# Performance work log

Hardware: AMD Instinct MI355X
Metric: run time of the kernel (lower is better)

Reference implementation:

```python
import jax, jax.numpy as jnp
import numpy as np

B, C, H, W = 2, 512, 32, 32
HEADS = 8      # attention heads
GROUPS = 8     # offset groups (defaults to heads)
DH = 64        # dim_head
DF = 4         # downsample_factor
OFF_SCALE = 4.0
EPS = 1e-5


def _bn(t, gamma, beta):
    # eval-mode BatchNorm2d with running_mean=0, running_var=1
    s = gamma / jnp.sqrt(1.0 + EPS)
    return t * s[None, :, None, None] + beta[None, :, None, None]


def _gconv1x1(t, w):
    # grouped 1x1 conv (bias-free); w: (GROUPS, out_per_group, in_per_group)
    b, c, h, ww = t.shape
    o = jnp.einsum('bgci,goc->bgoi', t.reshape(b, GROUPS, c // GROUPS, h * ww), w)
    return o.reshape(b, GROUPS * w.shape[1], h, ww)


def _grid_sample(img, grid):
    # F.grid_sample: bilinear, padding_mode='zeros', align_corners=False
    # img: (N,Ci,Hi,Wi); grid: (N,Hg,Wg,2), grid[...,0]=x, grid[...,1]=y in [-1,1]
    N, Ci, Hi, Wi = img.shape
    gx = (grid[..., 0] + 1.0) * (Wi / 2.0) - 0.5
    gy = (grid[..., 1] + 1.0) * (Hi / 2.0) - 0.5
    x0 = jnp.floor(gx)
    y0 = jnp.floor(gy)
    wx = gx - x0
    wy = gy - y0

    def gather(im, ix, iy):
        valid = (ix >= 0) & (ix < Wi) & (iy >= 0) & (iy < Hi)
        ixc = jnp.clip(ix, 0, Wi - 1).astype(jnp.int32)
        iyc = jnp.clip(iy, 0, Hi - 1).astype(jnp.int32)
        return im[:, iyc, ixc] * valid[None].astype(im.dtype)

    def sample_one(im, x0, y0, wx, wy):
        v00 = gather(im, x0, y0)
        v01 = gather(im, x0 + 1, y0)
        v10 = gather(im, x0, y0 + 1)
        v11 = gather(im, x0 + 1, y0 + 1)
        wx = wx[None]
        wy = wy[None]
        return (v00 * (1 - wx) * (1 - wy) + v01 * wx * (1 - wy)
                + v10 * (1 - wx) * wy + v11 * wx * wy)

    return jax.vmap(sample_one)(img, x0, y0, wx, wy)


def _forward(x, bn1_g, bn1_b, bn2_g, bn2_b, qw, kw, vw, out_w, out_b,
             off_dw_w, off_dw_b, off_pw_w,
             cpb_w1, cpb_b1, cpb_w2, cpb_b2, cpb_w3, cpb_b3,
             mlp_w1, mlp_b1, mlp_w2, mlp_b2):
    b = x.shape[0]
    xn = _bn(x, bn1_g, bn1_b)
    # ---- deformable attention ----
    q = _gconv1x1(xn, qw)                                   # (b, 512, H, W)
    qg = q.reshape(b * GROUPS, DH, H, W)
    # to_offsets: depthwise conv k=6, s=4, p=1 -> GELU -> 1x1(64->2) -> tanh * offset_scale
    off = jax.lax.conv_general_dilated(
        qg, off_dw_w, (DF, DF), ((1, 1), (1, 1)),
        dimension_numbers=('NCHW', 'OIHW', 'NCHW'), feature_group_count=DH)
    off = jax.nn.gelu(off + off_dw_b[None, :, None, None], approximate=False)
    off = jnp.tanh(jnp.einsum('bchw,oc->bohw', off, off_pw_w)) * OFF_SCALE   # (b*G, 2, Hd, Wd)
    Hd, Wd = off.shape[-2], off.shape[-1]
    gy, gx = jnp.meshgrid(jnp.arange(Hd, dtype=x.dtype), jnp.arange(Wd, dtype=x.dtype), indexing='ij')
    vx = gx[None] + off[:, 0]
    vy = gy[None] + off[:, 1]
    # normalize_grid (lucidrains): first comp by (Hd-1), second by (Wd-1)
    nx = 2.0 * vx / max(Hd - 1, 1) - 1.0
    ny = 2.0 * vy / max(Wd - 1, 1) - 1.0
    vgrid_scaled = jnp.stack((nx, ny), axis=-1)             # (b*G, Hd, Wd, 2)
    kv = _grid_sample(xn.reshape(b * GROUPS, DH, H, W), vgrid_scaled)
    kv = kv.reshape(b, GROUPS * DH, Hd, Wd)
    k = _gconv1x1(kv, kw)
    v = _gconv1x1(kv, vw)
    scale = DH ** -0.5
    qh = q.reshape(b, HEADS, DH, H * W).transpose(0, 1, 3, 2) * scale    # (b,h,i,d)
    kh = k.reshape(b, HEADS, DH, Hd * Wd).transpose(0, 1, 3, 2)          # (b,h,j,d)
    vh = v.reshape(b, HEADS, DH, Hd * Wd).transpose(0, 1, 3, 2)
    # continuous relative position bias (CPB)
    qgy, qgx = jnp.meshgrid(jnp.arange(H, dtype=x.dtype), jnp.arange(W, dtype=x.dtype), indexing='ij')
    grid_q = jnp.stack((2.0 * qgx / max(H - 1, 1) - 1.0,
                        2.0 * qgy / max(W - 1, 1) - 1.0), axis=-1).reshape(1, H * W, 2)
    grid_kv = vgrid_scaled.reshape(b * GROUPS, Hd * Wd, 2)
    pos = grid_q[:, :, None, :] - grid_kv[:, None, :, :]    # (b*G, i, j, 2)
    bias = jnp.sign(pos) * jnp.log1p(jnp.abs(pos))
    bias = jax.nn.relu(bias @ cpb_w1 + cpb_b1)
    bias = jax.nn.relu(bias @ cpb_w2 + cpb_b2)
    bias = (bias @ cpb_w3 + cpb_b3).reshape(b, GROUPS, H * W, Hd * Wd)   # heads//groups == 1
    sim = jnp.einsum('bhid,bhjd->bhij', qh, kh) + bias
    attn = jax.nn.softmax(sim, axis=-1)
    out = jnp.einsum('bhij,bhjd->bhid', attn, vh)
    out = out.transpose(0, 1, 3, 2).reshape(b, HEADS * DH, H, W)
    out = jnp.einsum('bchw,oc->bohw', out, out_w) + out_b[None, :, None, None]
    x = x + out
    # ---- conv1x1 MLP ----
    xn2 = _bn(x, bn2_g, bn2_b)
    h1 = jax.nn.gelu(jnp.einsum('bchw,oc->bohw', xn2, mlp_w1) + mlp_b1[None, :, None, None],
                     approximate=False)
    return x + jnp.einsum('bchw,oc->bohw', h1, mlp_w2) + mlp_b2[None, :, None, None]


def setup_inputs():
    ks = jax.random.split(jax.random.key(0), 16)
    w = lambda k, shape: jax.random.normal(k, shape, dtype=jnp.float32) * 0.02
    return {
        'x': jax.random.normal(ks[0], (B, C, H, W), dtype=jnp.float32),
        'bn1_g': jnp.ones((C,), jnp.float32),
        'bn1_b': jnp.zeros((C,), jnp.float32),
        'bn2_g': jnp.ones((C,), jnp.float32),
        'bn2_b': jnp.zeros((C,), jnp.float32),
        'qw': w(ks[1], (GROUPS, DH, C // GROUPS)),
        'kw': w(ks[2], (GROUPS, DH, C // GROUPS)),
        'vw': w(ks[3], (GROUPS, DH, C // GROUPS)),
        'out_w': w(ks[4], (C, HEADS * DH)),
        'out_b': jnp.zeros((C,), jnp.float32),
        'off_dw_w': w(ks[5], (DH, 1, 6, 6)),
        'off_dw_b': jnp.zeros((DH,), jnp.float32),
        'off_pw_w': w(ks[6], (2, DH)),
        'cpb_w1': w(ks[7], (2, 128)),
        'cpb_b1': jnp.zeros((128,), jnp.float32),
        'cpb_w2': w(ks[8], (128, 128)),
        'cpb_b2': jnp.zeros((128,), jnp.float32),
        'cpb_w3': w(ks[9], (128, 1)),
        'cpb_b3': jnp.zeros((1,), jnp.float32),
        'mlp_w1': w(ks[10], (4 * C, C)),
        'mlp_b1': jnp.zeros((4 * C,), jnp.float32),
        'mlp_w2': w(ks[11], (C, 4 * C)),
        'mlp_b2': jnp.zeros((C,), jnp.float32),
    }


def reference(x, bn1_g, bn1_b, bn2_g, bn2_b, qw, kw, vw, out_w, out_b,
              off_dw_w, off_dw_b, off_pw_w,
              cpb_w1, cpb_b1, cpb_w2, cpb_b2, cpb_w3, cpb_b3,
              mlp_w1, mlp_b1, mlp_w2, mlp_b2):
    return _forward(x, bn1_g, bn1_b, bn2_g, bn2_b, qw, kw, vw, out_w, out_b,
                    off_dw_w, off_dw_b, off_pw_w,
                    cpb_w1, cpb_b1, cpb_w2, cpb_b2, cpb_w3, cpb_b3,
                    mlp_w1, mlp_b1, mlp_w2, mlp_b2)
```

## Files before the change

kernel.cpp:

```cpp
#include <hip/hip_runtime.h>
#include <hip/hip_bf16.h>
#include <math.h>

#define BB 2
#define CC 512
#define HH 32
#define WW 32
#define HWP 1024
#define GG 8
#define DH 64
#define HD 8
#define WD 8
#define JJ 64
#define BG 16
#define EPS 1e-5f

typedef __attribute__((ext_vector_type(8))) short short8;
typedef __attribute__((ext_vector_type(4))) short s16x4;
typedef __attribute__((ext_vector_type(4))) float f32x4;
typedef __attribute__((ext_vector_type(4))) unsigned short u16x4;
typedef __attribute__((ext_vector_type(4))) unsigned int u32x4;

static __device__ __forceinline__ short f2bf(float x) {
    unsigned u = __builtin_bit_cast(unsigned, x);
    u += 0x7FFFu + ((u >> 16) & 1u);
    return (short)(u >> 16);
}
static __device__ __forceinline__ float bf2f(unsigned short h) {
    return __builtin_bit_cast(float, (unsigned)h << 16);
}

__global__ void k_wpack(const float* __restrict__ qw, const float* __restrict__ ow,
                        const float* __restrict__ w1, const float* __restrict__ w2,
                        const float* __restrict__ cw2, unsigned short* __restrict__ wp,
                        unsigned short* __restrict__ w2p) {
    int idx = blockIdx.x * 256 + threadIdx.x;
    if (idx < 2392064) {
        float v;
        if (idx < 32768) v = qw[idx];
        else if (idx < 294912) v = ow[idx - 32768];
        else if (idx < 1343488) v = w1[idx - 294912];
        else v = w2[idx - 1343488];
        wp[idx] = (unsigned short)f2bf(v);
    } else if (idx < 2408448) {
        int i2 = idx - 2392064;
        int k = i2 >> 7, n = i2 & 127;
        int dest = ((((n >> 4) * 4 + (k >> 5)) * 64) + (((k >> 3) & 3) * 16) + (n & 15)) * 8 + (k & 7);
        w2p[dest] = (unsigned short)f2bf(cw2[i2]);
    }
}

__global__ __launch_bounds__(256) void k_qgemm(
    const float* __restrict__ x, const float* __restrict__ g1,
    const float* __restrict__ b1, const unsigned short* __restrict__ qwp,
    unsigned short* __restrict__ qt) {
    __shared__ __align__(16) short As[64][72];
    __shared__ __align__(16) short Bs[64][72];
    int blk = blockIdx.x;
    int bg = blk >> 4, nt = blk & 15;
    int b = bg >> 3, g = bg & 7;
    int i0 = nt * 64;
    int tid = threadIdx.x, lane = tid & 63, wv = tid >> 6;
    int wm = (wv >> 1) * 32, wn = (wv & 1) * 32;
    int l15 = lane & 15, quad = lane >> 4;
    const float invs = 1.0f / sqrtf(1.0f + EPS);
    {
        int c4 = (tid & 15) * 4;
        int ob = tid >> 4;
#pragma unroll
        for (int p = 0; p < 4; p++) {
            int o = ob + p * 16;
            u16x4 v = *(const u16x4*)(qwp + (size_t)(g * 64 + o) * 64 + c4);
            *(u16x4*)&As[o][c4] = v;
        }
    }
    {
        int i4 = (tid & 15) * 4;
        int cb = tid >> 4;
#pragma unroll
        for (int p = 0; p < 4; p++) {
            int c = cb + p * 16;
            f32x4 v = *(const f32x4*)(x + (size_t)(b * CC + g * 64 + c) * HWP + i0 + i4);
            float sc = g1[g * 64 + c] * invs;
            float sh = b1[g * 64 + c];
            Bs[i4 + 0][c] = f2bf(fmaf(v.x, sc, sh));
            Bs[i4 + 1][c] = f2bf(fmaf(v.y, sc, sh));
            Bs[i4 + 2][c] = f2bf(fmaf(v.z, sc, sh));
            Bs[i4 + 3][c] = f2bf(fmaf(v.w, sc, sh));
        }
    }
    __syncthreads();
    f32x4 acc[2][2];
#pragma unroll
    for (int a = 0; a < 2; a++)
#pragma unroll
        for (int c = 0; c < 2; c++) acc[a][c] = (f32x4){0.f, 0.f, 0.f, 0.f};
#pragma unroll
    for (int ks = 0; ks < 2; ks++) {
        short8 af0 = *(const short8*)&As[wm + l15][ks * 32 + quad * 8];
        short8 af1 = *(const short8*)&As[wm + 16 + l15][ks * 32 + quad * 8];
        short8 bf0 = *(const short8*)&Bs[wn + l15][ks * 32 + quad * 8];
        short8 bf1 = *(const short8*)&Bs[wn + 16 + l15][ks * 32 + quad * 8];
        acc[0][0] = __builtin_amdgcn_mfma_f32_16x16x32_bf16(af0, bf0, acc[0][0], 0, 0, 0);
        acc[0][1] = __builtin_amdgcn_mfma_f32_16x16x32_bf16(af0, bf1, acc[0][1], 0, 0, 0);
        acc[1][0] = __builtin_amdgcn_mfma_f32_16x16x32_bf16(af1, bf0, acc[1][0], 0, 0, 0);
        acc[1][1] = __builtin_amdgcn_mfma_f32_16x16x32_bf16(af1, bf1, acc[1][1], 0, 0, 0);
    }
    __syncthreads();
#pragma unroll
    for (int im = 0; im < 2; im++)
#pragma unroll
        for (int r = 0; r < 4; r++) {
            int m = wm + im * 16 + quad * 4 + r;
#pragma unroll
            for (int in_ = 0; in_ < 2; in_++) {
                int n = wn + in_ * 16 + l15;
                As[n][m] = f2bf(acc[im][in_][r]);
            }
        }
    __syncthreads();
    {
        int n = tid >> 2;
        int c0 = (tid & 3) * 16;
        short8 a = *(const short8*)&As[n][c0];
        short8 c = *(const short8*)&As[n][c0 + 8];
        unsigned short* dst = qt + ((size_t)bg * 1024 + i0 + n) * 64 + c0;
        *(short8*)dst = a;
        *(short8*)(dst + 8) = c;
    }
}

__global__ __launch_bounds__(64) void k_offskv(
    const unsigned short* __restrict__ qt, const float* __restrict__ dww,
    const float* __restrict__ dwb, const float* __restrict__ pw,
    const float* __restrict__ x, const float* __restrict__ g1,
    const float* __restrict__ b1, const float* __restrict__ kw,
    const float* __restrict__ vw, float* __restrict__ vgrid,
    float* __restrict__ kk, float* __restrict__ vv) {
    __shared__ float sm[64];
    int blk = blockIdx.x;
    int bg = blk >> 6;
    int hd = (blk >> 3) & 7;
    int wd = blk & 7;
    int g = bg & 7, b = bg >> 3;
    int ch = threadIdx.x;
    const unsigned short* qb = qt + (size_t)bg * 65536;
    float acc = 0.f;
#pragma unroll
    for (int kh = 0; kh < 6; kh++) {
        int hin = hd * 4 - 1 + kh;
        if (hin < 0 || hin >= HH) continue;
#pragma unroll
        for (int kw_ = 0; kw_ < 6; kw_++) {
            int win = wd * 4 - 1 + kw_;
            if (win < 0 || win >= WW) continue;
            acc = fmaf(bf2f(qb[(hin * WW + win) * 64 + ch]), dww[ch * 36 + kh * 6 + kw_], acc);
        }
    }
    acc += dwb[ch];
    float ge = 0.5f * acc * (1.0f + erff(acc * 0.7071067811865475f));
    float p0 = ge * pw[ch];
    float p1 = ge * pw[64 + ch];
#pragma unroll
    for (int off = 32; off; off >>= 1) {
        p0 += __shfl_xor(p0, off);
        p1 += __shfl_xor(p1, off);
    }
    float nx = 2.0f * ((float)wd + tanhf(p0) * 4.0f) / 7.0f - 1.0f;
    float ny = 2.0f * ((float)hd + tanhf(p1) * 4.0f) / 7.0f - 1.0f;
    if (ch == 0) {
        vgrid[blk * 2] = nx;
        vgrid[blk * 2 + 1] = ny;
    }
    {
        int cg = g * 64 + ch;
        const float invs = 1.0f / sqrtf(1.0f + EPS);
        float s = g1[cg] * invs;
        float bv = b1[cg];
        float gx = (nx + 1.0f) * 16.0f - 0.5f;
        float gy = (ny + 1.0f) * 16.0f - 0.5f;
        float x0f = floorf(gx), y0f = floorf(gy);
        float wx = gx - x0f, wy = gy - y0f;
        int x0 = (int)x0f, y0 = (int)y0f;
        const float* im = x + (size_t)(b * CC + cg) * HWP;
        float sx = 0.f, sw = 0.f;
        float w00 = (1 - wx) * (1 - wy), w01 = wx * (1 - wy);
        float w10 = (1 - wx) * wy, w11 = wx * wy;
        if (x0 >= 0 && x0 < WW && y0 >= 0 && y0 < HH)                 { sx += w00 * im[y0 * WW + x0];           sw += w00; }
        if (x0 + 1 >= 0 && x0 + 1 < WW && y0 >= 0 && y0 < HH)         { sx += w01 * im[y0 * WW + x0 + 1];       sw += w01; }
        if (x0 >= 0 && x0 < WW && y0 + 1 >= 0 && y0 + 1 < HH)         { sx += w10 * im[(y0 + 1) * WW + x0];     sw += w10; }
        if (x0 + 1 >= 0 && x0 + 1 < WW && y0 + 1 >= 0 && y0 + 1 < HH) { sx += w11 * im[(y0 + 1) * WW + x0 + 1]; sw += w11; }
        sm[ch] = s * sx + bv * sw;
    }
    __syncthreads();
    int j = blk & 63;
    const float* kwr = kw + (size_t)(g * 64 + ch) * 64;
    const float* vwr = vw + (size_t)(g * 64 + ch) * 64;
    float ak = 0.f, av = 0.f;
#pragma unroll
    for (int c = 0; c < 64; c++) {
        float tv = sm[c];
        ak = fmaf(tv, kwr[c], ak);
        av = fmaf(tv, vwr[c], av);
    }
    kk[(size_t)bg * 4096 + j * 64 + ch] = ak;
    vv[(size_t)bg * 4096 + j * 64 + ch] = av;
}

__global__ __launch_bounds__(256) void k_cpb(
    const float* __restrict__ vgrid, const unsigned short* __restrict__ w2p,
    const float* __restrict__ w1, const float* __restrict__ b1,
    const float* __restrict__ b2, const float* __restrict__ w3,
    const float* __restrict__ b3, float* __restrict__ bias) {
    __shared__ __align__(16) short w2fs[16384];
    int tid = threadIdx.x;
    {
        const u32x4* src = (const u32x4*)w2p;
        u32x4* dst = (u32x4*)w2fs;
        for (int c = tid; c < 2048; c += 256) dst[c] = src[c];
    }
    float bias3 = b3[0];
    __syncthreads();

    int lane = tid & 63;
    int wv = tid >> 6;
    int l15 = lane & 15;
    int quad = lane >> 4;

#pragma unroll 1
    for (int it = 0; it < 4; it++) {
        int p = (blockIdx.x * 4 + it) * 4 + wv;
        int cofs = (int)((unsigned)p >> 20);
        int bg = p >> 11;
        int i = (p >> 1) & 1023;
        int jbase = (p & 1) * 32;
        int hi = i >> 5, wi = i & 31;
        float qx = 2.0f * (float)wi / 31.0f - 1.0f;
        float qy = 2.0f * (float)hi / 31.0f - 1.0f;

        int jA = jbase + l15;
        float gkxA = vgrid[(bg * 64 + jA) * 2];
        float gkyA = vgrid[(bg * 64 + jA) * 2 + 1];
        float gkxB = vgrid[(bg * 64 + jA + 16) * 2];
        float gkyB = vgrid[(bg * 64 + jA + 16) * 2 + 1];
        float p0 = qx - gkxA, p1 = qy - gkyA;
        float s0a = copysignf(log1pf(fabsf(p0)), p0);
        float s1a = copysignf(log1pf(fabsf(p1)), p1);
        p0 = qx - gkxB; p1 = qy - gkyB;
        float s0b = copysignf(log1pf(fabsf(p0)), p0);
        float s1b = copysignf(log1pf(fabsf(p1)), p1);

        short8 hA[4], hB[4];
#pragma unroll
        for (int kc = 0; kc < 4; kc++) {
            f32x4 cu0 = *(const f32x4*)(w1 + cofs + kc * 32 + quad * 8);
            f32x4 cu1 = *(const f32x4*)(w1 + cofs + kc * 32 + quad * 8 + 4);
            f32x4 cv0 = *(const f32x4*)(w1 + cofs + 128 + kc * 32 + quad * 8);
            f32x4 cv1 = *(const f32x4*)(w1 + cofs + 128 + kc * 32 + quad * 8 + 4);
            f32x4 cb0 = *(const f32x4*)(b1 + cofs + kc * 32 + quad * 8);
            f32x4 cb1 = *(const f32x4*)(b1 + cofs + kc * 32 + quad * 8 + 4);
            u32x4 pa, pb;
#pragma unroll
            for (int j2 = 0; j2 < 4; j2++) {
                int e0 = 2 * j2, e1 = 2 * j2 + 1;
                float u0 = (e0 < 4) ? cu0[e0] : cu1[e0 - 4];
                float u1 = (e1 < 4) ? cu0[e1] : cu1[e1 - 4];
                float v0 = (e0 < 4) ? cv0[e0] : cv1[e0 - 4];
                float v1 = (e1 < 4) ? cv0[e1] : cv1[e1 - 4];
                float c0 = (e0 < 4) ? cb0[e0] : cb1[e0 - 4];
                float c1 = (e1 < 4) ? cb0[e1] : cb1[e1 - 4];
                unsigned a0 = __builtin_bit_cast(unsigned,
                    fmaxf(fmaf(s0a, u0, fmaf(s1a, v0, c0)), 0.f)) + 0x8000u;
                unsigned a1 = __builtin_bit_cast(unsigned,
                    fmaxf(fmaf(s0a, u1, fmaf(s1a, v1, c1)), 0.f)) + 0x8000u;
                pa[j2] = __builtin_amdgcn_perm(a1, a0, 0x07060302);
                unsigned b0 = __builtin_bit_cast(unsigned,
                    fmaxf(fmaf(s0b, u0, fmaf(s1b, v0, c0)), 0.f)) + 0x8000u;
                unsigned b1_ = __builtin_bit_cast(unsigned,
                    fmaxf(fmaf(s0b, u1, fmaf(s1b, v1, c1)), 0.f)) + 0x8000u;
                pb[j2] = __builtin_amdgcn_perm(b1_, b0, 0x07060302);
            }
            hA[kc] = __builtin_bit_cast(short8, pa);
            hB[kc] = __builtin_bit_cast(short8, pb);
        }

        float psumA = 0.f, psumB = 0.f;
#pragma unroll 2
        for (int nt = 0; nt < 8; nt++) {
            f32x4 accA = (f32x4){0.f, 0.f, 0.f, 0.f};
            f32x4 accB = (f32x4){0.f, 0.f, 0.f, 0.f};
#pragma unroll
            for (int kc = 0; kc < 4; kc++) {
                short8 af = *(const short8*)(w2fs + (((nt * 4 + kc) * 64) + lane) * 8);
                accA = __builtin_amdgcn_mfma_f32_16x16x32_bf16(af, hA[kc], accA, 0, 0, 0);
                accB = __builtin_amdgcn_mfma_f32_16x16x32_bf16(af, hB[kc], accB, 0, 0, 0);
            }
            f32x4 b2q = *(const f32x4*)(b2 + cofs + nt * 16 + quad * 4);
            f32x4 w3q = *(const f32x4*)(w3 + cofs + nt * 16 + quad * 4);
#pragma unroll
            for (int r = 0; r < 4; r++) {
                psumA = fmaf(fmaxf(accA[r] + b2q[r], 0.f), w3q[r], psumA);
                psumB = fmaf(fmaxf(accB[r] + b2q[r], 0.f), w3q[r], psumB);
            }
        }
        psumA += __shfl_xor(psumA, 16);
        psumA += __shfl_xor(psumA, 32);
        psumB += __shfl_xor(psumB, 16);
        psumB += __shfl_xor(psumB, 32);
        if (quad == 0) {
            bias[(size_t)(p * 2 + 0) * 16 + l15] = psumA + bias3;
            bias[(size_t)(p * 2 + 1) * 16 + l15] = psumB + bias3;
        }
    }
}

__global__ __launch_bounds__(256) void k_attn(
    const unsigned short* __restrict__ qt, const float* __restrict__ kk,
    const float* __restrict__ vv, const float* __restrict__ bias,
    unsigned short* __restrict__ ao) {
    __shared__ __align__(16) short Ks[64][72];
    __shared__ __align__(16) short Vt[64][72];
    __shared__ __align__(16) short Qs[64][72];
    __shared__ __align__(16) short Ps[4][16][72];
    int blk = blockIdx.x;
    int bg = blk >> 4;
    int chunk = blk & 15;
    int i0 = chunk * 64;
    int b = bg >> 3, g = bg & 7;
    int tid = threadIdx.x, lane = tid & 63, wv = tid >> 6;
    int l15 = lane & 15, quad = lane >> 4;

    const float* kbase = kk + (size_t)bg * 4096;
    const float* vbase = vv + (size_t)bg * 4096;
#pragma unroll
    for (int it = 0; it < 4; it++) {
        int e4 = it * 1024 + tid * 4;
        int j = e4 >> 6, d = e4 & 63;
        f32x4 k4 = *(const f32x4*)(kbase + e4);
        s16x4 s = {f2bf(k4.x), f2bf(k4.y), f2bf(k4.z), f2bf(k4.w)};
        *(s16x4*)&Ks[j][d] = s;
        f32x4 v4 = *(const f32x4*)(vbase + e4);
        Vt[d + 0][j] = f2bf(v4.x);
        Vt[d + 1][j] = f2bf(v4.y);
        Vt[d + 2][j] = f2bf(v4.z);
        Vt[d + 3][j] = f2bf(v4.w);
    }
    {
        const unsigned short* qtb = qt + ((size_t)bg * 1024 + i0) * 64;
#pragma unroll
        for (int it = 0; it < 4; it++) {
            int e4 = it * 1024 + tid * 4;
            int i = e4 >> 6, d = e4 & 63;
            u16x4 v = *(const u16x4*)(qtb + e4);
            *(u16x4*)&Qs[i][d] = v;
        }
    }
    __syncthreads();

    int iw = wv * 16;
    f32x4 Sacc[4];
#pragma unroll
    for (int nt = 0; nt < 4; nt++) Sacc[nt] = (f32x4){0.f, 0.f, 0.f, 0.f};
#pragma unroll
    for (int ks = 0; ks < 2; ks++) {
        short8 aq = *(const short8*)&Qs[iw + l15][quad * 8 + ks * 32];
#pragma unroll
        for (int nt = 0; nt < 4; nt++) {
            short8 bk = *(const short8*)&Ks[nt * 16 + l15][quad * 8 + ks * 32];
            Sacc[nt] = __builtin_amdgcn_mfma_f32_16x16x32_bf16(aq, bk, Sacc[nt], 0, 0, 0);
        }
    }
    const float* bp = bias + ((size_t)bg * 1024 + i0 + iw + quad * 4) * 64 + l15;
    float Sv[4][4];
#pragma unroll
    for (int nt = 0; nt < 4; nt++)
#pragma unroll
        for (int r = 0; r < 4; r++)
            Sv[nt][r] = fmaf(Sacc[nt][r], 0.125f, bp[r * 64 + nt * 16]);
#pragma unroll
    for (int r = 0; r < 4; r++) {
        float m = fmaxf(fmaxf(Sv[0][r], Sv[1][r]), fmaxf(Sv[2][r], Sv[3][r]));
        m = fmaxf(m, __shfl_xor(m, 1));
        m = fmaxf(m, __shfl_xor(m, 2));
        m = fmaxf(m, __shfl_xor(m, 4));
        m = fmaxf(m, __shfl_xor(m, 8));
        float l = 0.f;
#pragma unroll
        for (int nt = 0; nt < 4; nt++) { Sv[nt][r] = expf(Sv[nt][r] - m); l += Sv[nt][r]; }
        l += __shfl_xor(l, 1);
        l += __shfl_xor(l, 2);
        l += __shfl_xor(l, 4);
        l += __shfl_xor(l, 8);
        float inv = 1.0f / l;
#pragma unroll
        for (int nt = 0; nt < 4; nt++)
            Ps[wv][quad * 4 + r][nt * 16 + l15] = f2bf(Sv[nt][r] * inv);
    }
    f32x4 Oacc[4];
#pragma unroll
    for (int nt = 0; nt < 4; nt++) Oacc[nt] = (f32x4){0.f, 0.f, 0.f, 0.f};
#pragma unroll
    for (int ks = 0; ks < 2; ks++) {
        short8 ap = *(const short8*)&Ps[wv][l15][quad * 8 + ks * 32];
#pragma unroll
        for (int nt = 0; nt < 4; nt++) {
            short8 bv = *(const short8*)&Vt[nt * 16 + l15][quad * 8 + ks * 32];
            Oacc[nt] = __builtin_amdgcn_mfma_f32_16x16x32_bf16(ap, bv, Oacc[nt], 0, 0, 0);
        }
    }
    __syncthreads();
#pragma unroll
    for (int nt = 0; nt < 4; nt++) {
        s16x4 o4 = {f2bf(Oacc[nt][0]), f2bf(Oacc[nt][1]), f2bf(Oacc[nt][2]), f2bf(Oacc[nt][3])};
        *(s16x4*)&Qs[nt * 16 + l15][iw + quad * 4] = o4;
    }
    __syncthreads();
    {
        int d = tid >> 2;
        int ic = (tid & 3) * 16;
        short8 a = *(const short8*)&Qs[d][ic];
        short8 c = *(const short8*)&Qs[d][ic + 8];
        unsigned short* dst = ao + (size_t)(b * CC + g * 64 + d) * HWP + i0 + ic;
        *(short8*)dst = a;
        *(short8*)(dst + 8) = c;
    }
}

template<int EPI, int KD, int BK, int MT>
__global__ __launch_bounds__(256) void k_gemm(
    const unsigned short* __restrict__ A, const unsigned short* __restrict__ Bh,
    const float* __restrict__ resid, const float* __restrict__ bias,
    void* __restrict__ outp, unsigned short* __restrict__ out2,
    const float* __restrict__ bns, const float* __restrict__ bnb) {
    constexpr int MM = MT * 64;
    __shared__ __align__(16) short As[64][BK + 8];
    __shared__ __align__(16) short Bs[64][BK + 8];
    int tid = threadIdx.x;
    int blk = blockIdx.x;
    int mt = blk & (MT - 1);
    int nb = blk / MT;
    int bb = nb >> 4, nt = nb & 15;
    int m0 = mt * 64, i0 = nt * 64;
    int lane = tid & 63, wv = tid >> 6;
    int wm = (wv >> 1) * 32, wn = (wv & 1) * 32;
    int l15 = lane & 15, quad = lane >> 4;
    const unsigned short* Af = A + (size_t)m0 * KD;
    const float invs = 1.0f / sqrtf(1.0f + EPS);

    f32x4 acc[2][2];
#pragma unroll
    for (int a = 0; a < 2; a++)
#pragma unroll
        for (int c = 0; c < 2; c++) acc[a][c] = (f32x4){0.f, 0.f, 0.f, 0.f};

    for (int k0 = 0; k0 < KD; k0 += BK) {
        __syncthreads();
        {
            int kk4 = (tid & (BK / 4 - 1)) * 4;
            int myb = tid / (BK / 4);
            constexpr int RP = 256 / (BK / 4);
#pragma unroll
            for (int p = 0; p < 64 / RP; p++) {
                int my = myb + p * RP;
                u16x4 v = *(const u16x4*)(Af + (size_t)my * KD + k0 + kk4);
                *(u16x4*)&As[my][kk4] = v;
            }
        }
        {
            int i4 = (tid & 15) * 4;
            int kyb = tid >> 4;
#pragma unroll
            for (int p = 0; p < BK / 16; p++) {
                int ky = kyb + p * 16;
                size_t goff = (size_t)bb * KD * HWP + (size_t)(k0 + ky) * HWP + i0 + i4;
                u16x4 v = *(const u16x4*)(Bh + goff);
                Bs[i4 + 0][ky] = (short)v.x;
                Bs[i4 + 1][ky] = (short)v.y;
                Bs[i4 + 2][ky] = (short)v.z;
                Bs[i4 + 3][ky] = (short)v.w;
            }
        }
        __syncthreads();
#pragma unroll
        for (int ks = 0; ks < BK / 32; ks++) {
            short8 af0 = *(const short8*)&As[wm + l15][ks * 32 + quad * 8];
            short8 af1 = *(const short8*)&As[wm + 16 + l15][ks * 32 + quad * 8];
            short8 bf0 = *(const short8*)&Bs[wn + l15][ks * 32 + quad * 8];
            short8 bf1 = *(const short8*)&Bs[wn + 16 + l15][ks * 32 + quad * 8];
            acc[0][0] = __builtin_amdgcn_mfma_f32_16x16x32_bf16(af0, bf0, acc[0][0], 0, 0, 0);
            acc[0][1] = __builtin_amdgcn_mfma_f32_16x16x32_bf16(af0, bf1, acc[0][1], 0, 0, 0);
            acc[1][0] = __builtin_amdgcn_mfma_f32_16x16x32_bf16(af1, bf0, acc[1][0], 0, 0, 0);
            acc[1][1] = __builtin_amdgcn_mfma_f32_16x16x32_bf16(af1, bf1, acc[1][1], 0, 0, 0);
        }
    }

    float* outF = (float*)outp;
    unsigned short* outH = (unsigned short*)outp;
#pragma unroll
    for (int im = 0; im < 2; im++) {
#pragma unroll
        for (int r = 0; r < 4; r++) {
            int m = m0 + wm + im * 16 + quad * 4 + r;
            float bv = bias[m];
#pragma unroll
            for (int in_ = 0; in_ < 2; in_++) {
                int n = i0 + wn + in_ * 16 + l15;
                size_t idx = ((size_t)bb * MM + m) * HWP + n;
                float v = acc[im][in_][r] + bv;
                if constexpr (EPI == 1) {
                    float ge = 0.5f * v * (1.0f + erff(v * 0.7071067811865475f));
                    outH[idx] = (unsigned short)f2bf(ge);
                } else if constexpr (EPI == 3) {
                    float vr = v + resid[idx];
                    outF[idx] = vr;
                    out2[idx] = (unsigned short)f2bf(fmaf(vr, bns[m] * invs, bnb[m]));
                } else {
                    outF[idx] = v + resid[idx];
                }
            }
        }
    }
}

extern "C" void kernel_launch(void* const* d_in, const int* in_sizes, int n_in,
                              void* d_out, int out_size, void* d_ws, size_t ws_size,
                              hipStream_t stream) {
    const float* x      = (const float*)d_in[0];
    const float* bn1_g  = (const float*)d_in[1];
    const float* bn1_b  = (const float*)d_in[2];
    const float* bn2_g  = (const float*)d_in[3];
    const float* bn2_b  = (const float*)d_in[4];
    const float* qw     = (const float*)d_in[5];
    const float* kw     = (const float*)d_in[6];
    const float* vw     = (const float*)d_in[7];
    const float* out_w  = (const float*)d_in[8];
    const float* out_b  = (const float*)d_in[9];
    const float* off_dw_w = (const float*)d_in[10];
    const float* off_dw_b = (const float*)d_in[11];
    const float* off_pw_w = (const float*)d_in[12];
    const float* cpb_w1 = (const float*)d_in[13];
    const float* cpb_b1 = (const float*)d_in[14];
    const float* cpb_w2 = (const float*)d_in[15];
    const float* cpb_b2 = (const float*)d_in[16];
    const float* cpb_w3 = (const float*)d_in[17];
    const float* cpb_b3 = (const float*)d_in[18];
    const float* mlp_w1 = (const float*)d_in[19];
    const float* mlp_b1 = (const float*)d_in[20];
    const float* mlp_w2 = (const float*)d_in[21];
    const float* mlp_b2 = (const float*)d_in[22];

    float* ws = (float*)d_ws;
    unsigned short* qt = (unsigned short*)(ws + 1048576);
    float* vgrid = ws + 2097152;
    float* kk    = ws + 2164736;
    float* vv    = ws + 2230272;
    unsigned short* w2p = (unsigned short*)(ws + 2295808);
    unsigned short* ao  = (unsigned short*)(ws + 2312192);
    unsigned short* xn2 = (unsigned short*)(ws + 2836480);
    float* xo    = ws + 3360768;
    float* h1of  = ws + 4409344;
    float* biasb = h1of;
    unsigned short* h1o = (unsigned short*)h1of;
    unsigned short* wp  = (unsigned short*)(ws + 6506496);
    unsigned short* qwp  = wp;
    unsigned short* owp  = wp + 32768;
    unsigned short* w1p  = wp + 294912;
    unsigned short* w2mp = wp + 1343488;

    hipLaunchKernelGGL(k_wpack, dim3(9408), dim3(256), 0, stream,
                       qw, out_w, mlp_w1, mlp_w2, cpb_w2, wp, w2p);
    hipLaunchKernelGGL(k_qgemm, dim3(256), dim3(256), 0, stream, x, bn1_g, bn1_b, qwp, qt);
    hipLaunchKernelGGL(k_offskv, dim3(1024), dim3(64), 0, stream,
                       qt, off_dw_w, off_dw_b, off_pw_w, x, bn1_g, bn1_b, kw, vw,
                       vgrid, kk, vv);
    hipLaunchKernelGGL(k_cpb, dim3(2048), dim3(256), 0, stream,
                       vgrid, w2p, cpb_w1, cpb_b1, cpb_b2, cpb_w3, cpb_b3, biasb);
    hipLaunchKernelGGL(k_attn, dim3(256), dim3(256), 0, stream, qt, kk, vv, biasb, ao);
    k_gemm<3, 512, 128, 8><<<dim3(256), dim3(256), 0, stream>>>(
        owp, ao, x, out_b, xo, xn2, bn2_g, bn2_b);
    k_gemm<1, 512, 128, 32><<<dim3(1024), dim3(256), 0, stream>>>(
        w1p, xn2, nullptr, mlp_b1, h1o, nullptr, nullptr, nullptr);
    k_gemm<2, 2048, 128, 8><<<dim3(256), dim3(256), 0, stream>>>(
        w2mp, h1o, xo, mlp_b2, d_out, nullptr, nullptr, nullptr);
}
```

Baseline: 256.3 us.

## Fuse weight packing into q-GEMM, stage q rows in LDS, store bias as bf16

```diff
diff --git a/kernel.cpp b/kernel.cpp
--- a/kernel.cpp
+++ b/kernel.cpp
@@ -30,37 +30,36 @@
     return __builtin_bit_cast(float, (unsigned)h << 16);
 }
 
-__global__ void k_wpack(const float* __restrict__ qw, const float* __restrict__ ow,
-                        const float* __restrict__ w1, const float* __restrict__ w2,
-                        const float* __restrict__ cw2, unsigned short* __restrict__ wp,
-                        unsigned short* __restrict__ w2p) {
-    int idx = blockIdx.x * 256 + threadIdx.x;
-    if (idx < 2392064) {
-        float v;
-        if (idx < 32768) v = qw[idx];
-        else if (idx < 294912) v = ow[idx - 32768];
-        else if (idx < 1343488) v = w1[idx - 294912];
-        else v = w2[idx - 1343488];
-        wp[idx] = (unsigned short)f2bf(v);
-    } else if (idx < 2408448) {
-        int i2 = idx - 2392064;
-        int k = i2 >> 7, n = i2 & 127;
-        int dest = ((((n >> 4) * 4 + (k >> 5)) * 64) + (((k >> 3) & 3) * 16) + (n & 15)) * 8 + (k & 7);
-        w2p[dest] = (unsigned short)f2bf(cw2[i2]);
-    }
-}
-
 __global__ __launch_bounds__(256) void k_qgemm(
     const float* __restrict__ x, const float* __restrict__ g1,
-    const float* __restrict__ b1, const unsigned short* __restrict__ qwp,
+    const float* __restrict__ b1, const float* __restrict__ qw,
+    const float* __restrict__ ow, const float* __restrict__ w1,
+    const float* __restrict__ w2, const float* __restrict__ cw2,
+    unsigned short* __restrict__ wp, unsigned short* __restrict__ w2p,
     unsigned short* __restrict__ qt) {
     __shared__ __align__(16) short As[64][72];
     __shared__ __align__(16) short Bs[64][72];
+    int tid = threadIdx.x;
+    for (int idx = blockIdx.x * 256 + tid; idx < 2408448; idx += 65536) {
+        if (idx < 2392064) {
+            float v;
+            if (idx < 32768) v = qw[idx];
+            else if (idx < 294912) v = ow[idx - 32768];
+            else if (idx < 1343488) v = w1[idx - 294912];
+            else v = w2[idx - 1343488];
+            wp[idx] = (unsigned short)f2bf(v);
+        } else {
+            int i2 = idx - 2392064;
+            int k = i2 >> 7, n = i2 & 127;
+            int dest = ((((n >> 4) * 4 + (k >> 5)) * 64) + (((k >> 3) & 3) * 16) + (n & 15)) * 8 + (k & 7);
+            w2p[dest] = (unsigned short)f2bf(cw2[i2]);
+        }
+    }
     int blk = blockIdx.x;
     int bg = blk >> 4, nt = blk & 15;
     int b = bg >> 3, g = bg & 7;
     int i0 = nt * 64;
-    int tid = threadIdx.x, lane = tid & 63, wv = tid >> 6;
+    int lane = tid & 63, wv = tid >> 6;
     int wm = (wv >> 1) * 32, wn = (wv & 1) * 32;
     int l15 = lane & 15, quad = lane >> 4;
     const float invs = 1.0f / sqrtf(1.0f + EPS);
@@ -70,8 +69,9 @@
 #pragma unroll
         for (int p = 0; p < 4; p++) {
             int o = ob + p * 16;
-            u16x4 v = *(const u16x4*)(qwp + (size_t)(g * 64 + o) * 64 + c4);
-            *(u16x4*)&As[o][c4] = v;
+            f32x4 v = *(const f32x4*)(qw + (size_t)(g * 64 + o) * 64 + c4);
+            s16x4 s = {f2bf(v.x), f2bf(v.y), f2bf(v.z), f2bf(v.w)};
+            *(s16x4*)&As[o][c4] = s;
         }
     }
     {
@@ -130,21 +130,32 @@
     }
 }
 
-__global__ __launch_bounds__(64) void k_offskv(
+__global__ __launch_bounds__(512) void k_offskv(
     const unsigned short* __restrict__ qt, const float* __restrict__ dww,
     const float* __restrict__ dwb, const float* __restrict__ pw,
     const float* __restrict__ x, const float* __restrict__ g1,
     const float* __restrict__ b1, const float* __restrict__ kw,
     const float* __restrict__ vw, float* __restrict__ vgrid,
     float* __restrict__ kk, float* __restrict__ vv) {
-    __shared__ float sm[64];
+    __shared__ __align__(16) short qs[6][2048];
+    __shared__ float sm[8][64];
     int blk = blockIdx.x;
-    int bg = blk >> 6;
-    int hd = (blk >> 3) & 7;
-    int wd = blk & 7;
+    int bg = blk >> 3, hd = blk & 7;
     int g = bg & 7, b = bg >> 3;
-    int ch = threadIdx.x;
-    const unsigned short* qb = qt + (size_t)bg * 65536;
+    int tid = threadIdx.x;
+    int wd = tid >> 6, ch = tid & 63;
+    {
+        const unsigned short* qb = qt + (size_t)bg * 65536;
+#pragma unroll
+        for (int r = 0; r < 6; r++) {
+            int hin = hd * 4 - 1 + r;
+            if (hin >= 0 && hin < HH) {
+                u16x4 v = *(const u16x4*)(qb + hin * 2048 + tid * 4);
+                *(u16x4*)&qs[r][tid * 4] = v;
+            }
+        }
+    }
+    __syncthreads();
     float acc = 0.f;
 #pragma unroll
     for (int kh = 0; kh < 6; kh++) {
@@ -154,7 +165,7 @@
         for (int kw_ = 0; kw_ < 6; kw_++) {
             int win = wd * 4 - 1 + kw_;
             if (win < 0 || win >= WW) continue;
-            acc = fmaf(bf2f(qb[(hin * WW + win) * 64 + ch]), dww[ch * 36 + kh * 6 + kw_], acc);
+            acc = fmaf(bf2f(qs[kh][win * 64 + ch]), dww[ch * 36 + kh * 6 + kw_], acc);
         }
     }
     acc += dwb[ch];
@@ -166,11 +177,12 @@
         p0 += __shfl_xor(p0, off);
         p1 += __shfl_xor(p1, off);
     }
+    int j = hd * 8 + wd;
     float nx = 2.0f * ((float)wd + tanhf(p0) * 4.0f) / 7.0f - 1.0f;
     float ny = 2.0f * ((float)hd + tanhf(p1) * 4.0f) / 7.0f - 1.0f;
     if (ch == 0) {
-        vgrid[blk * 2] = nx;
-        vgrid[blk * 2 + 1] = ny;
+        vgrid[(bg * 64 + j) * 2] = nx;
+        vgrid[(bg * 64 + j) * 2 + 1] = ny;
     }
     {
         int cg = g * 64 + ch;
@@ -190,16 +202,15 @@
         if (x0 + 1 >= 0 && x0 + 1 < WW && y0 >= 0 && y0 < HH)         { sx += w01 * im[y0 * WW + x0 + 1];       sw += w01; }
         if (x0 >= 0 && x0 < WW && y0 + 1 >= 0 && y0 + 1 < HH)         { sx += w10 * im[(y0 + 1) * WW + x0];     sw += w10; }
         if (x0 + 1 >= 0 && x0 + 1 < WW && y0 + 1 >= 0 && y0 + 1 < HH) { sx += w11 * im[(y0 + 1) * WW + x0 + 1]; sw += w11; }
-        sm[ch] = s * sx + bv * sw;
-    }
-    __syncthreads();
-    int j = blk & 63;
+        sm[wd][ch] = s * sx + bv * sw;
+    }
+    __syncthreads();
     const float* kwr = kw + (size_t)(g * 64 + ch) * 64;
     const float* vwr = vw + (size_t)(g * 64 + ch) * 64;
     float ak = 0.f, av = 0.f;
 #pragma unroll
     for (int c = 0; c < 64; c++) {
-        float tv = sm[c];
+        float tv = sm[wd][c];
         ak = fmaf(tv, kwr[c], ak);
         av = fmaf(tv, vwr[c], av);
     }
@@ -211,7 +222,7 @@
     const float* __restrict__ vgrid, const unsigned short* __restrict__ w2p,
     const float* __restrict__ w1, const float* __restrict__ b1,
     const float* __restrict__ b2, const float* __restrict__ w3,
-    const float* __restrict__ b3, float* __restrict__ bias) {
+    const float* __restrict__ b3, unsigned short* __restrict__ bias) {
     __shared__ __align__(16) short w2fs[16384];
     int tid = threadIdx.x;
     {
@@ -308,15 +319,15 @@
         psumB += __shfl_xor(psumB, 16);
         psumB += __shfl_xor(psumB, 32);
         if (quad == 0) {
-            bias[(size_t)(p * 2 + 0) * 16 + l15] = psumA + bias3;
-            bias[(size_t)(p * 2 + 1) * 16 + l15] = psumB + bias3;
+            bias[(size_t)(p * 2 + 0) * 16 + l15] = (unsigned short)f2bf(psumA + bias3);
+            bias[(size_t)(p * 2 + 1) * 16 + l15] = (unsigned short)f2bf(psumB + bias3);
         }
     }
 }
 
 __global__ __launch_bounds__(256) void k_attn(
     const unsigned short* __restrict__ qt, const float* __restrict__ kk,
-    const float* __restrict__ vv, const float* __restrict__ bias,
+    const float* __restrict__ vv, const unsigned short* __restrict__ bias,
     unsigned short* __restrict__ ao) {
     __shared__ __align__(16) short Ks[64][72];
     __shared__ __align__(16) short Vt[64][72];
@@ -370,13 +381,13 @@
             Sacc[nt] = __builtin_amdgcn_mfma_f32_16x16x32_bf16(aq, bk, Sacc[nt], 0, 0, 0);
         }
     }
-    const float* bp = bias + ((size_t)bg * 1024 + i0 + iw + quad * 4) * 64 + l15;
+    const unsigned short* bp = bias + ((size_t)bg * 1024 + i0 + iw + quad * 4) * 64 + l15;
     float Sv[4][4];
 #pragma unroll
     for (int nt = 0; nt < 4; nt++)
 #pragma unroll
         for (int r = 0; r < 4; r++)
-            Sv[nt][r] = fmaf(Sacc[nt][r], 0.125f, bp[r * 64 + nt * 16]);
+            Sv[nt][r] = fmaf(Sacc[nt][r], 0.125f, bf2f(bp[r * 64 + nt * 16]));
 #pragma unroll
     for (int r = 0; r < 4; r++) {
         float m = fmaxf(fmaxf(Sv[0][r], Sv[1][r]), fmaxf(Sv[2][r], Sv[3][r]));
@@ -559,18 +570,16 @@
     unsigned short* xn2 = (unsigned short*)(ws + 2836480);
     float* xo    = ws + 3360768;
     float* h1of  = ws + 4409344;
-    float* biasb = h1of;
+    unsigned short* biasb = (unsigned short*)h1of;
     unsigned short* h1o = (unsigned short*)h1of;
     unsigned short* wp  = (unsigned short*)(ws + 6506496);
-    unsigned short* qwp  = wp;
     unsigned short* owp  = wp + 32768;
     unsigned short* w1p  = wp + 294912;
     unsigned short* w2mp = wp + 1343488;
 
-    hipLaunchKernelGGL(k_wpack, dim3(9408), dim3(256), 0, stream,
-                       qw, out_w, mlp_w1, mlp_w2, cpb_w2, wp, w2p);
-    hipLaunchKernelGGL(k_qgemm, dim3(256), dim3(256), 0, stream, x, bn1_g, bn1_b, qwp, qt);
-    hipLaunchKernelGGL(k_offskv, dim3(1024), dim3(64), 0, stream,
+    hipLaunchKernelGGL(k_qgemm, dim3(256), dim3(256), 0, stream,
+                       x, bn1_g, bn1_b, qw, out_w, mlp_w1, mlp_w2, cpb_w2, wp, w2p, qt);
+    hipLaunchKernelGGL(k_offskv, dim3(128), dim3(512), 0, stream,
                        qt, off_dw_w, off_dw_b, off_pw_w, x, bn1_g, bn1_b, kw, vw,
                        vgrid, kk, vv);
     hipLaunchKernelGGL(k_cpb, dim3(2048), dim3(256), 0, stream,
```

New measurement: 270.2 us. +5.4%, slower.

## Prefetch next GEMM K-tile into registers and store attention bias as bf16

Applied to the files above, without the earlier changes.

```diff
diff --git a/kernel.cpp b/kernel.cpp
--- a/kernel.cpp
+++ b/kernel.cpp
@@ -211,7 +211,7 @@
     const float* __restrict__ vgrid, const unsigned short* __restrict__ w2p,
     const float* __restrict__ w1, const float* __restrict__ b1,
     const float* __restrict__ b2, const float* __restrict__ w3,
-    const float* __restrict__ b3, float* __restrict__ bias) {
+    const float* __restrict__ b3, unsigned short* __restrict__ bias) {
     __shared__ __align__(16) short w2fs[16384];
     int tid = threadIdx.x;
     {
@@ -308,15 +308,15 @@
         psumB += __shfl_xor(psumB, 16);
         psumB += __shfl_xor(psumB, 32);
         if (quad == 0) {
-            bias[(size_t)(p * 2 + 0) * 16 + l15] = psumA + bias3;
-            bias[(size_t)(p * 2 + 1) * 16 + l15] = psumB + bias3;
+            bias[(size_t)(p * 2 + 0) * 16 + l15] = (unsigned short)f2bf(psumA + bias3);
+            bias[(size_t)(p * 2 + 1) * 16 + l15] = (unsigned short)f2bf(psumB + bias3);
         }
     }
 }
 
 __global__ __launch_bounds__(256) void k_attn(
     const unsigned short* __restrict__ qt, const float* __restrict__ kk,
-    const float* __restrict__ vv, const float* __restrict__ bias,
+    const float* __restrict__ vv, const unsigned short* __restrict__ bias,
     unsigned short* __restrict__ ao) {
     __shared__ __align__(16) short Ks[64][72];
     __shared__ __align__(16) short Vt[64][72];
@@ -370,13 +370,13 @@
             Sacc[nt] = __builtin_amdgcn_mfma_f32_16x16x32_bf16(aq, bk, Sacc[nt], 0, 0, 0);
         }
     }
-    const float* bp = bias + ((size_t)bg * 1024 + i0 + iw + quad * 4) * 64 + l15;
+    const unsigned short* bp = bias + ((size_t)bg * 1024 + i0 + iw + quad * 4) * 64 + l15;
     float Sv[4][4];
 #pragma unroll
     for (int nt = 0; nt < 4; nt++)
 #pragma unroll
         for (int r = 0; r < 4; r++)
-            Sv[nt][r] = fmaf(Sacc[nt][r], 0.125f, bp[r * 64 + nt * 16]);
+            Sv[nt][r] = fmaf(Sacc[nt][r], 0.125f, bf2f(bp[r * 64 + nt * 16]));
 #pragma unroll
     for (int r = 0; r < 4; r++) {
         float m = fmaxf(fmaxf(Sv[0][r], Sv[1][r]), fmaxf(Sv[2][r], Sv[3][r]));
@@ -433,6 +433,10 @@
     void* __restrict__ outp, unsigned short* __restrict__ out2,
     const float* __restrict__ bns, const float* __restrict__ bnb) {
     constexpr int MM = MT * 64;
+    constexpr int KV4 = BK / 4;
+    constexpr int RP = 256 / KV4;
+    constexpr int NA = 64 / RP;
+    constexpr int NB = BK / 16;
     __shared__ __align__(16) short As[64][BK + 8];
     __shared__ __align__(16) short Bs[64][BK + 8];
     int tid = threadIdx.x;
@@ -446,41 +450,48 @@
     int l15 = lane & 15, quad = lane >> 4;
     const unsigned short* Af = A + (size_t)m0 * KD;
     const float invs = 1.0f / sqrtf(1.0f + EPS);
+    int kk4 = (tid & (KV4 - 1)) * 4;
+    int myb = tid / KV4;
+    int i4 = (tid & 15) * 4;
+    int kyb = tid >> 4;
 
     f32x4 acc[2][2];
 #pragma unroll
     for (int a = 0; a < 2; a++)
 #pragma unroll
         for (int c = 0; c < 2; c++) acc[a][c] = (f32x4){0.f, 0.f, 0.f, 0.f};
+
+    u16x4 ra[NA], rb[NB];
+#pragma unroll
+    for (int p = 0; p < NA; p++)
+        ra[p] = *(const u16x4*)(Af + (size_t)(myb + p * RP) * KD + kk4);
+#pragma unroll
+    for (int p = 0; p < NB; p++)
+        rb[p] = *(const u16x4*)(Bh + (size_t)bb * KD * HWP + (size_t)(kyb + p * 16) * HWP + i0 + i4);
 
     for (int k0 = 0; k0 < KD; k0 += BK) {
         __syncthreads();
-        {
-            int kk4 = (tid & (BK / 4 - 1)) * 4;
-            int myb = tid / (BK / 4);
-            constexpr int RP = 256 / (BK / 4);
-#pragma unroll
-            for (int p = 0; p < 64 / RP; p++) {
-                int my = myb + p * RP;
-                u16x4 v = *(const u16x4*)(Af + (size_t)my * KD + k0 + kk4);
-                *(u16x4*)&As[my][kk4] = v;
-            }
-        }
-        {
-            int i4 = (tid & 15) * 4;
-            int kyb = tid >> 4;
-#pragma unroll
-            for (int p = 0; p < BK / 16; p++) {
-                int ky = kyb + p * 16;
-                size_t goff = (size_t)bb * KD * HWP + (size_t)(k0 + ky) * HWP + i0 + i4;
-                u16x4 v = *(const u16x4*)(Bh + goff);
-                Bs[i4 + 0][ky] = (short)v.x;
-                Bs[i4 + 1][ky] = (short)v.y;
-                Bs[i4 + 2][ky] = (short)v.z;
-                Bs[i4 + 3][ky] = (short)v.w;
-            }
+#pragma unroll
+        for (int p = 0; p < NA; p++)
+            *(u16x4*)&As[myb + p * RP][kk4] = ra[p];
+#pragma unroll
+        for (int p = 0; p < NB; p++) {
+            int ky = kyb + p * 16;
+            Bs[i4 + 0][ky] = (short)rb[p].x;
+            Bs[i4 + 1][ky] = (short)rb[p].y;
+            Bs[i4 + 2][ky] = (short)rb[p].z;
+            Bs[i4 + 3][ky] = (short)rb[p].w;
         }
         __syncthreads();
+        int kn = k0 + BK;
+        if (kn < KD) {
+#pragma unroll
+            for (int p = 0; p < NA; p++)
+                ra[p] = *(const u16x4*)(Af + (size_t)(myb + p * RP) * KD + kn + kk4);
+#pragma unroll
+            for (int p = 0; p < NB; p++)
+                rb[p] = *(const u16x4*)(Bh + (size_t)bb * KD * HWP + (size_t)(kn + kyb + p * 16) * HWP + i0 + i4);
+        }
 #pragma unroll
         for (int ks = 0; ks < BK / 32; ks++) {
             short8 af0 = *(const short8*)&As[wm + l15][ks * 32 + quad * 8];
@@ -559,7 +570,7 @@
     unsigned short* xn2 = (unsigned short*)(ws + 2836480);
     float* xo    = ws + 3360768;
     float* h1of  = ws + 4409344;
-    float* biasb = h1of;
+    unsigned short* biasb = (unsigned short*)h1of;
     unsigned short* h1o = (unsigned short*)h1of;
     unsigned short* wp  = (unsigned short*)(ws + 6506496);
     unsigned short* qwp  = wp;
```

After: 255.6 us. Within noise of the previous version (-0.3%).
